# Kernel optimization log

Hardware: AMD Instinct MI355X
Metric: run time of the kernel (lower is better)

Reference implementation:

```python
import jax, jax.numpy as jnp
import numpy as np

N_HOS, N_TYPES = 8, 16
N_COMBOS = N_HOS * N_TYPES          # 128
N_STRUCTS = 512
BATCH = 2048
HID = 20
N_ITERS = 60                        # PDHG iterations (fixed, jit-friendly)
CONTROL = 10.0                      # control_strength in the original module


def _spectral_bound(S):
    # ||[S; I]||_2^2 = lambda_max(S^T S + I) via power iteration (S is constant).
    v = jnp.ones((S.shape[1],), S.dtype)
    def pit(v, _):
        u = S.T @ (S @ v) + v
        return u / jnp.linalg.norm(u), None
    v, _ = jax.lax.scan(pit, v, None, length=30)
    return jnp.sqrt(v @ (S.T @ (S @ v) + v))


def _solve_lp(S, b, z):
    """Batched solve of: max 1^T x - CONTROL*||x - z||_2  s.t. x >= 0, S x <= b.
    Chambolle-Pock PDHG with K = [S; -I], f(x) = -1^T x + CONTROL*||x - z||.
    S: [m, n]; b: [B, m]; z: [B, n] -> x: [B, n].
    """
    B, m = b.shape
    n = z.shape[1]
    L = _spectral_bound(S)
    tau = 0.9 / L
    sig = 0.9 / L
    w = jnp.ones((n,), z.dtype)     # LP objective weights (module uses ones)

    x = jnp.maximum(z, 0.0)
    xb = x
    lam1 = jnp.zeros((B, m), z.dtype)   # duals for S x <= b
    lam2 = jnp.zeros((B, n), z.dtype)   # duals for x >= 0 (lam2 <= 0 form)

    def step(carry, _):
        x, xb, lam1, lam2 = carry
        # dual ascent: prox of conjugates of the constraint indicators
        u1 = lam1 + sig * (xb @ S.T)                 # [B, m]
        lam1 = jnp.maximum(u1 - sig * b, 0.0)
        lam2 = jnp.minimum(lam2 + sig * xb, 0.0)
        # primal: prox of tau*(-w^T x + CONTROL*||x - z||): block soft-threshold
        v = x - tau * (lam1 @ S + lam2)
        u = v + tau * w - z
        nrm = jnp.linalg.norm(u, axis=1, keepdims=True)
        scale = jnp.maximum(0.0, 1.0 - tau * CONTROL / jnp.maximum(nrm, 1e-12))
        x_new = z + scale * u
        xb = 2.0 * x_new - x
        return (x_new, xb, lam1, lam2), None

    (x, _, _, _), _ = jax.lax.scan(step, (x, xb, lam1, lam2), None, length=N_ITERS)
    return x


def _mlp(Xf, W1, b1, W2, b2, W3, b3, W4, b4):
    h = jnp.tanh(Xf @ W1 + b1)
    h = jnp.tanh(h @ W2 + b2)
    h = jnp.tanh(h @ W3 + b3)
    return h @ W4 + b4


def setup_inputs() -> dict:
    key = jax.random.key(0)
    ks = jax.random.split(key, 10)
    X = jax.random.uniform(ks[0], (BATCH, N_HOS, N_TYPES), jnp.float32)
    # 0/1 cycle-incidence matrix, ~4 nonzeros per column (cycles of length ~4)
    S = jax.random.bernoulli(ks[1], 4.0 / N_COMBOS, (N_COMBOS, N_STRUCTS)).astype(jnp.float32)
    def lin(k, fi, fo):
        return jax.random.normal(k, (fi, fo), jnp.float32) / jnp.sqrt(fi)
    W1 = lin(ks[2], N_COMBOS, HID); b1 = jnp.zeros((HID,), jnp.float32)
    W2 = lin(ks[3], HID, HID);      b2 = jnp.zeros((HID,), jnp.float32)
    W3 = lin(ks[4], HID, HID);      b3 = jnp.zeros((HID,), jnp.float32)
    W4 = lin(ks[5], HID, N_STRUCTS); b4 = jnp.zeros((N_STRUCTS,), jnp.float32)
    return {"X": X, "W1": W1, "b1": b1, "W2": W2, "b2": b2, "W3": W3,
            "b3": b3, "W4": W4, "b4": b4, "S": S, "batch_size": BATCH}


def reference(X, W1, b1, W2, b2, W3, b3, W4, b4, S, batch_size):
    Xf = X.reshape(batch_size, N_COMBOS)       # bids, also the LP rhs b
    z = _mlp(Xf, W1, b1, W2, b2, W3, b3, W4, b4)   # [B, n_structures]
    return _solve_lp(S, Xf, z)                 # allocation x1 [B, n_structures]
```

## Files before the change

### kernel.cpp

```cpp
#include <hip/hip_runtime.h>


#define NC    128
#define NS    512
#define BATCH 2048
#define HID   20

typedef unsigned int  uint;
typedef unsigned short ushort;
typedef float v2f __attribute__((ext_vector_type(2)));


template <int CTRL, int RMASK = 0xf>
__device__ __forceinline__ float dppadd(float s) {
    return s + __builtin_bit_cast(float,
        __builtin_amdgcn_update_dpp(0, __builtin_bit_cast(int, s), CTRL, RMASK, 0xf, true));
}
__device__ __forceinline__ float quad_sum(float s) {
    s = dppadd<0xB1>(s);
    s = dppadd<0x4E>(s);
    return s;
}
__device__ __forceinline__ float wave_sum_bcast(float x) {
    float s = x;
    s = dppadd<0x111>(s);
    s = dppadd<0x112>(s);
    s = dppadd<0x114>(s);
    s = dppadd<0x118>(s);
    s = dppadd<0x142, 0xa>(s);
    s = dppadd<0x143, 0xc>(s);
    return __builtin_bit_cast(float, __builtin_amdgcn_readlane(__builtin_bit_cast(int, s), 63));
}
__device__ __forceinline__ v2f vfma(v2f a, v2f b, v2f c) { return __builtin_elementwise_fma(a, b, c); }
__device__ __forceinline__ v2f vmax0(v2f a) { const v2f z = {0.f, 0.f}; return __builtin_elementwise_max(a, z); }
__device__ __forceinline__ v2f vmin0(v2f a) { const v2f z = {0.f, 0.f}; return __builtin_elementwise_min(a, z); }

__global__ __launch_bounds__(512) void prep_scan(
    const float* __restrict__ S, uint* __restrict__ colmask_g, uint* __restrict__ rowbits_g)
{
    __shared__ uint mcol[NS];
    const int t = threadIdx.x, g = blockIdx.x;
    float vals[32];
#pragma unroll
    for (int j = 0; j < 32; ++j) vals[j] = S[(g * 32 + j) * NS + t];
    uint m = 0;
#pragma unroll
    for (int j = 0; j < 32; ++j) if (vals[j] != 0.0f) m |= (1u << j);
    mcol[t] = m;
    colmask_g[t * 4 + g] = m;
    __syncthreads();
    const int j = t >> 4, w = t & 15;
    uint val = 0;
#pragma unroll
    for (int c = 0; c < 32; ++c)
        val |= (((mcol[w * 32 + c] >> j) & 1u) << c);
    rowbits_g[(g * 32 + j) * 16 + w] = val;
}

__global__ __launch_bounds__(512) void prep_finish(
    const uint* __restrict__ colmask_g, const uint* __restrict__ rowbits_g,
    float* __restrict__ tau_ws,
    uint* __restrict__ col_meta, uint* __restrict__ col_cnt_g,
    uint* __restrict__ row_meta, uint* __restrict__ row_cnt_g)
{
    __shared__ ushort clist[NS][16];
    __shared__ ushort rql[NS][10];
    __shared__ int    ccnt_l[NS];
    __shared__ int    rcnt_l[NS];
    __shared__ float  u_lds[NS + 1];
    __shared__ float  sv_lds[NC];
    __shared__ float  red_pi[32];
    const int t = threadIdx.x;

    uint cm[4];
    { const uint4 c4 = *(const uint4*)&colmask_g[t * 4];
      cm[0] = c4.x; cm[1] = c4.y; cm[2] = c4.z; cm[3] = c4.w; }
    {
        int cc = 0;
#pragma unroll
        for (int g = 0; g < 4; ++g) {
            uint m = cm[g];
            while (m) {
                const int b = __ffs(m) - 1; m &= m - 1;
                if (cc < 16) clist[t][cc] = (ushort)((g * 32 + b) * 8);
                ++cc;
            }
        }
        if (cc > 16) cc = 16;
        const int cc2 = (cc + 1) & ~1;
        for (int k = cc; k < 16; ++k) clist[t][k] = (ushort)(NC * 8);
        ccnt_l[t] = cc2;
    }
    if (t < NC) {
#pragma unroll
        for (int q = 0; q < 4; ++q)
            for (int p = 0; p < 10; ++p) rql[t * 4 + q][p] = (ushort)(NS * 8);
        uint rb[16];
        { const uint4 a = *(const uint4*)&rowbits_g[t * 16];
          const uint4 b = *(const uint4*)&rowbits_g[t * 16 + 4];
          const uint4 c = *(const uint4*)&rowbits_g[t * 16 + 8];
          const uint4 d = *(const uint4*)&rowbits_g[t * 16 + 12];
          rb[0]=a.x; rb[1]=a.y; rb[2]=a.z;  rb[3]=a.w;  rb[4]=b.x;  rb[5]=b.y;  rb[6]=b.z;  rb[7]=b.w;
          rb[8]=c.x; rb[9]=c.y; rb[10]=c.z; rb[11]=c.w; rb[12]=d.x; rb[13]=d.y; rb[14]=d.z; rb[15]=d.w; }
        int e = 0;
#pragma unroll
        for (int w = 0; w < 16; ++w) {
            uint m = rb[w];
            while (m) {
                const int b = __ffs(m) - 1; m &= m - 1;
                const int q = e & 3, p = e >> 2;
                if (p < 10) rql[t * 4 + q][p] = (ushort)((w * 32 + b) * 8);
                ++e;
            }
        }
#pragma unroll
        for (int q = 0; q < 4; ++q) {
            int n = (e - q + 3) >> 2;
            if (n < 0) n = 0;
            if (n > 10) n = 10;
            rcnt_l[t * 4 + q] = (n + 1) & ~1;
        }
    }
    if (t == 0) u_lds[NS] = 0.0f;
    if (t < 32) red_pi[t] = 0.0f;
    u_lds[t] = 1.0f;
    __syncthreads();

    {
        col_cnt_g[t] = (uint)ccnt_l[t];
#pragma unroll
        for (int k = 0; k < 16; ++k) col_meta[t * 16 + k] = (uint)clist[t][k];
        row_cnt_g[t] = (uint)rcnt_l[t];
#pragma unroll
        for (int k = 0; k < 12; ++k)
            row_meta[t * 12 + k] = (k < 10) ? (uint)rql[t][k] : (uint)(NS * 8);
    }

    const int rcn = rcnt_l[t];
    float u_loc = 1.0f;
    for (int it = 0; it <= 30; ++it) {
        const float inv = it ? rsqrtf(red_pi[it - 1]) : 1.0f;
        float s = 0.0f;
        for (int k = 0; k < rcn; ++k) {
            const uint a = rql[t][k];
            s += *(const float*)((const char*)u_lds + (a >> 1));
        }
        s = quad_sum(s * inv);
        if ((t & 3) == 3) sv_lds[t >> 2] = s;
        __syncthreads();
        const float vt = u_loc * inv;
        float w = vt;
#pragma unroll
        for (int g = 0; g < 4; ++g) {
            uint m = cm[g];
            while (m) { const int b = __ffs(m) - 1; m &= m - 1; w += sv_lds[g * 32 + b]; }
        }
        float p = (it < 30) ? w * w : w * vt;
        p = wave_sum_bcast(p);
        if ((t & 63) == 0) atomicAdd(&red_pi[it], p);
        u_lds[t] = w;
        u_loc = w;
        __syncthreads();
    }
    if (t == 0) tau_ws[0] = 0.9f / sqrtf(red_pi[30]);
}

__global__ __launch_bounds__(512, 8) void solve_kernel(
    const float* __restrict__ X,
    const float* __restrict__ W1, const float* __restrict__ b1,
    const float* __restrict__ W2, const float* __restrict__ b2,
    const float* __restrict__ W3, const float* __restrict__ b3,
    const float* __restrict__ W4, const float* __restrict__ b4,
    const float* __restrict__ tau_ws,
    const uint* __restrict__ col_meta, const uint* __restrict__ col_cnt_g,
    const uint* __restrict__ row_meta, const uint* __restrict__ row_cnt_g,
    float* __restrict__ out)
{
    __shared__ alignas(16) float2 xb_lds[NS + 1];
    __shared__ alignas(16) float2 lam1_lds[NC + 1];
    __shared__ alignas(16) float2 redslot[8];
    __shared__ alignas(16) float2 b_lds[NC];
    __shared__ float ha[2][HID], hb[2][HID];

    const int t  = threadIdx.x;
    const int r0 = blockIdx.x * 2, r1 = r0 + 1;

    uint4 cA, cB, cC, cD, rA, rB, rC;
    { const uint4* g = (const uint4*)&col_meta[t * 16];
      cA = g[0]; cB = g[1]; cC = g[2]; cD = g[3]; }
    { const uint4* g = (const uint4*)&row_meta[t * 12];
      rA = g[0]; rB = g[1]; rC = g[2]; }
    const int ccn = (int)col_cnt_g[t];
    const int rcn = (int)row_cnt_g[t];

    if (t == 0) { xb_lds[NS] = make_float2(0.f, 0.f); lam1_lds[NC] = make_float2(0.f, 0.f); }
    if (t < NC) b_lds[t] = make_float2(X[r0 * NC + t], X[r1 * NC + t]);
    __syncthreads();

    if (t < 2 * HID) {
        const int rr = t >= HID, tt = t - rr * HID;
        float s = b1[tt];
        for (int k = 0; k < NC; ++k)
            s = fmaf(rr ? b_lds[k].y : b_lds[k].x, W1[k * HID + tt], s);
        ha[rr][tt] = tanhf(s);
    }
    __syncthreads();
    if (t < 2 * HID) {
        const int rr = t >= HID, tt = t - rr * HID;
        float s = b2[tt];
        for (int k = 0; k < HID; ++k) s = fmaf(ha[rr][k], W2[k * HID + tt], s);
        hb[rr][tt] = tanhf(s);
    }
    __syncthreads();
    if (t < 2 * HID) {
        const int rr = t >= HID, tt = t - rr * HID;
        float s = b3[tt];
        for (int k = 0; k < HID; ++k) s = fmaf(hb[rr][k], W3[k * HID + tt], s);
        ha[rr][tt] = tanhf(s);
    }
    __syncthreads();
    float z0 = b4[t], z1 = z0;
    for (int h = 0; h < HID; ++h) {
        const float w = W4[h * NS + t];
        z0 = fmaf(ha[0][h], w, z0);
        z1 = fmaf(ha[1][h], w, z1);
    }

    const float tau = tau_ws[0];
    const float c10 = 10.0f * tau;
    const v2f tauv = {tau, tau};
    const v2f sigv = tauv;
    const int r = t >> 2, q = t & 3;
    const v2f bb = {b_lds[r].x, b_lds[r].y};

    const v2f z = {z0, z1};
    v2f x  = vmax0(z);
    v2f xb = x;
    v2f u  = {0.f, 0.f};
    v2f l1 = {0.f, 0.f};
    v2f l2 = vmin0(sigv * xb);
    xb_lds[t] = make_float2(xb.x, xb.y);
    __syncthreads();

    const char* xbB = (const char*)xb_lds;
    const char* lmB = (const char*)lam1_lds;
    for (int it = 0; it < 60; ++it) {
        v2f s = {0.f, 0.f};
        s += *(const v2f*)(xbB + rA.x);
        s += *(const v2f*)(xbB + rA.y);
        if (rcn > 2) {
            s += *(const v2f*)(xbB + rA.z);
            s += *(const v2f*)(xbB + rA.w);
            if (rcn > 4) {
                s += *(const v2f*)(xbB + rB.x);
                s += *(const v2f*)(xbB + rB.y);
                if (rcn > 6) {
                    s += *(const v2f*)(xbB + rB.z);
                    s += *(const v2f*)(xbB + rB.w);
                    if (rcn > 8) {
                        s += *(const v2f*)(xbB + rC.x);
                        s += *(const v2f*)(xbB + rC.y);
                    }
                }
            }
        }
        const v2f sq = {quad_sum(s.x), quad_sum(s.y)};
        l1 = vmax0(vfma(sigv, sq - bb, l1));
        if (q == 3) lam1_lds[r] = make_float2(l1.x, l1.y);
        __syncthreads();
        v2f s2 = {0.f, 0.f};
        s2 += *(const v2f*)(lmB + cA.x);
        s2 += *(const v2f*)(lmB + cA.y);
        if (ccn > 2) {
            s2 += *(const v2f*)(lmB + cA.z);
            s2 += *(const v2f*)(lmB + cA.w);
            if (ccn > 4) {
                s2 += *(const v2f*)(lmB + cB.x);
                s2 += *(const v2f*)(lmB + cB.y);
                if (ccn > 6) {
                    s2 += *(const v2f*)(lmB + cB.z);
                    s2 += *(const v2f*)(lmB + cB.w);
                    if (ccn > 8) {
                        s2 += *(const v2f*)(lmB + cC.x);
                        s2 += *(const v2f*)(lmB + cC.y);
                        if (ccn > 10) {
                            s2 += *(const v2f*)(lmB + cC.z);
                            s2 += *(const v2f*)(lmB + cC.w);
                            if (ccn > 12) {
                                s2 += *(const v2f*)(lmB + cD.x);
                                s2 += *(const v2f*)(lmB + cD.y);
                                if (ccn > 14) {
                                    s2 += *(const v2f*)(lmB + cD.z);
                                    s2 += *(const v2f*)(lmB + cD.w);
                                }
                            }
                        }
                    }
                }
            }
        }
        const v2f v = x - tauv * (s2 + l2);
        u = (v + tauv) - z;
        const v2f p = u * u;
        const float p0 = wave_sum_bcast(p.x);
        const float p1 = wave_sum_bcast(p.y);
        if ((t & 63) == 0) redslot[t >> 6] = make_float2(p0, p1);
        __syncthreads();
        const float4* rs = (const float4*)redslot;
        const float4 Ra = rs[0], Rb = rs[1], Rc = rs[2], Rd = rs[3];
        const v2f tot = (((v2f){Ra.x, Ra.y} + (v2f){Ra.z, Ra.w}) +
                         ((v2f){Rb.x, Rb.y} + (v2f){Rb.z, Rb.w})) +
                        (((v2f){Rc.x, Rc.y} + (v2f){Rc.z, Rc.w}) +
                         ((v2f){Rd.x, Rd.y} + (v2f){Rd.z, Rd.w}));
        const v2f sc = {fmaxf(0.f, 1.f - c10 * rsqrtf(tot.x)),
                        fmaxf(0.f, 1.f - c10 * rsqrtf(tot.y))};
        const v2f xn = vfma(sc, u, z);
        xb = (xn + xn) - x;
        x  = xn;
        l2 = vmin0(vfma(sigv, xb, l2));
        xb_lds[t] = make_float2(xb.x, xb.y);
        __syncthreads();
    }
    out[r0 * NS + t] = x.x;
    out[r1 * NS + t] = x.y;
}

extern "C" void kernel_launch(void* const* d_in, const int* in_sizes, int n_in,
                              void* d_out, int out_size, void* d_ws, size_t ws_size,
                              hipStream_t stream)
{
    const float* X  = (const float*)d_in[0];
    const float* W1 = (const float*)d_in[1];
    const float* b1 = (const float*)d_in[2];
    const float* W2 = (const float*)d_in[3];
    const float* b2 = (const float*)d_in[4];
    const float* W3 = (const float*)d_in[5];
    const float* b3 = (const float*)d_in[6];
    const float* W4 = (const float*)d_in[7];
    const float* b4 = (const float*)d_in[8];
    const float* S  = (const float*)d_in[9];
    float* out = (float*)d_out;

    char* ws = (char*)d_ws;
    float* tau_ws    = (float*)(ws + 0);
    uint*  colmask_g = (uint*)(ws + 64);
    uint*  rowbits_g = (uint*)(ws + 8256);
    uint*  col_meta  = (uint*)(ws + 16448);
    uint*  col_cnt_g = (uint*)(ws + 49216);
    uint*  row_meta  = (uint*)(ws + 51264);
    uint*  row_cnt_g = (uint*)(ws + 75840);

    prep_scan<<<4, 512, 0, stream>>>(S, colmask_g, rowbits_g);
    prep_finish<<<1, 512, 0, stream>>>(colmask_g, rowbits_g, tau_ws,
                                       col_meta, col_cnt_g, row_meta, row_cnt_g);
    solve_kernel<<<BATCH / 2, 512, 0, stream>>>(X, W1, b1, W2, b2, W3, b3, W4, b4,
                                                tau_ws, col_meta, col_cnt_g,
                                                row_meta, row_cnt_g, out);
}
```

Measured before the change: 280.1 us.

## Process four batch rows per block with float4 LDS gathers and padded layout

The solve kernel now handles four batch rows per 512-thread block instead of two. Each thread carries v4f state, so every gathered LDS index and every barrier is amortized over twice as many rows, and the launch uses half as many blocks. The LDS arrays are padded (one slot per 8 entries) and the byte offsets are re-encoded at 16-byte stride, likely to reduce bank conflicts on the wider loads. In exchange, register use roughly doubles, the occupancy hint drops from 8 to 4 blocks per CU, and the grid shrinks to 512 blocks, which leaves less parallelism for hiding latency.

```diff
diff --git a/kernel.cpp b/kernel.cpp
--- a/kernel.cpp
+++ b/kernel.cpp
@@ -8,7 +8,7 @@
 
 typedef unsigned int  uint;
 typedef unsigned short ushort;
-typedef float v2f __attribute__((ext_vector_type(2)));
+typedef float v4f __attribute__((ext_vector_type(4)));
 
 
 template <int CTRL, int RMASK = 0xf>
@@ -31,9 +31,12 @@
     s = dppadd<0x143, 0xc>(s);
     return __builtin_bit_cast(float, __builtin_amdgcn_readlane(__builtin_bit_cast(int, s), 63));
 }
-__device__ __forceinline__ v2f vfma(v2f a, v2f b, v2f c) { return __builtin_elementwise_fma(a, b, c); }
-__device__ __forceinline__ v2f vmax0(v2f a) { const v2f z = {0.f, 0.f}; return __builtin_elementwise_max(a, z); }
-__device__ __forceinline__ v2f vmin0(v2f a) { const v2f z = {0.f, 0.f}; return __builtin_elementwise_min(a, z); }
+__device__ __forceinline__ v4f quad_sum4(v4f s) {
+    return (v4f){quad_sum(s.x), quad_sum(s.y), quad_sum(s.z), quad_sum(s.w)};
+}
+__device__ __forceinline__ v4f vfma(v4f a, v4f b, v4f c) { return __builtin_elementwise_fma(a, b, c); }
+__device__ __forceinline__ v4f vmax0(v4f a) { const v4f z = {0.f,0.f,0.f,0.f}; return __builtin_elementwise_max(a, z); }
+__device__ __forceinline__ v4f vmin0(v4f a) { const v4f z = {0.f,0.f,0.f,0.f}; return __builtin_elementwise_min(a, z); }
 
 __global__ __launch_bounds__(512) void prep_scan(
     const float* __restrict__ S, uint* __restrict__ colmask_g, uint* __restrict__ rowbits_g)
@@ -67,7 +70,7 @@
     __shared__ ushort rql[NS][10];
     __shared__ int    ccnt_l[NS];
     __shared__ int    rcnt_l[NS];
-    __shared__ float  u_lds[NS + 1];
+    __shared__ float  u_lds[577];
     __shared__ float  sv_lds[NC];
     __shared__ float  red_pi[32];
     const int t = threadIdx.x;
@@ -82,19 +85,20 @@
             uint m = cm[g];
             while (m) {
                 const int b = __ffs(m) - 1; m &= m - 1;
-                if (cc < 16) clist[t][cc] = (ushort)((g * 32 + b) * 8);
+                const int i = g * 32 + b;
+                if (cc < 16) clist[t][cc] = (ushort)((i + (i >> 3)) * 16);
                 ++cc;
             }
         }
         if (cc > 16) cc = 16;
         const int cc2 = (cc + 1) & ~1;
-        for (int k = cc; k < 16; ++k) clist[t][k] = (ushort)(NC * 8);
+        for (int k = cc; k < 16; ++k) clist[t][k] = (ushort)(144 * 16);
         ccnt_l[t] = cc2;
     }
     if (t < NC) {
 #pragma unroll
         for (int q = 0; q < 4; ++q)
-            for (int p = 0; p < 10; ++p) rql[t * 4 + q][p] = (ushort)(NS * 8);
+            for (int p = 0; p < 10; ++p) rql[t * 4 + q][p] = (ushort)(576 * 16);
         uint rb[16];
         { const uint4 a = *(const uint4*)&rowbits_g[t * 16];
           const uint4 b = *(const uint4*)&rowbits_g[t * 16 + 4];
@@ -109,7 +113,8 @@
             while (m) {
                 const int b = __ffs(m) - 1; m &= m - 1;
                 const int q = e & 3, p = e >> 2;
-                if (p < 10) rql[t * 4 + q][p] = (ushort)((w * 32 + b) * 8);
+                const int j = w * 32 + b;
+                if (p < 10) rql[t * 4 + q][p] = (ushort)((j + (j >> 3)) * 16);
                 ++e;
             }
         }
@@ -121,9 +126,9 @@
             rcnt_l[t * 4 + q] = (n + 1) & ~1;
         }
     }
-    if (t == 0) u_lds[NS] = 0.0f;
+    if (t == 0) u_lds[576] = 0.0f;
     if (t < 32) red_pi[t] = 0.0f;
-    u_lds[t] = 1.0f;
+    u_lds[t + (t >> 3)] = 1.0f;
     __syncthreads();
 
     {
@@ -133,7 +138,7 @@
         row_cnt_g[t] = (uint)rcnt_l[t];
 #pragma unroll
         for (int k = 0; k < 12; ++k)
-            row_meta[t * 12 + k] = (k < 10) ? (uint)rql[t][k] : (uint)(NS * 8);
+            row_meta[t * 12 + k] = (k < 10) ? (uint)rql[t][k] : (uint)(576 * 16);
     }
 
     const int rcn = rcnt_l[t];
@@ -143,7 +148,7 @@
         float s = 0.0f;
         for (int k = 0; k < rcn; ++k) {
             const uint a = rql[t][k];
-            s += *(const float*)((const char*)u_lds + (a >> 1));
+            s += *(const float*)((const char*)u_lds + (a >> 2));
         }
         s = quad_sum(s * inv);
         if ((t & 3) == 3) sv_lds[t >> 2] = s;
@@ -158,14 +163,14 @@
         float p = (it < 30) ? w * w : w * vt;
         p = wave_sum_bcast(p);
         if ((t & 63) == 0) atomicAdd(&red_pi[it], p);
-        u_lds[t] = w;
+        u_lds[t + (t >> 3)] = w;
         u_loc = w;
         __syncthreads();
     }
     if (t == 0) tau_ws[0] = 0.9f / sqrtf(red_pi[30]);
 }
 
-__global__ __launch_bounds__(512, 8) void solve_kernel(
+__global__ __launch_bounds__(512, 4) void solve_kernel(
     const float* __restrict__ X,
     const float* __restrict__ W1, const float* __restrict__ b1,
     const float* __restrict__ W2, const float* __restrict__ b2,
@@ -176,14 +181,14 @@
     const uint* __restrict__ row_meta, const uint* __restrict__ row_cnt_g,
     float* __restrict__ out)
 {
-    __shared__ alignas(16) float2 xb_lds[NS + 1];
-    __shared__ alignas(16) float2 lam1_lds[NC + 1];
-    __shared__ alignas(16) float2 redslot[8];
-    __shared__ alignas(16) float2 b_lds[NC];
-    __shared__ float ha[2][HID], hb[2][HID];
+    __shared__ alignas(16) v4f xb_lds[577];
+    __shared__ alignas(16) v4f lam1_lds[145];
+    __shared__ alignas(16) v4f redslot[8];
+    __shared__ alignas(16) v4f b_lds[NC];
+    __shared__ float ha[4][HID], hb[4][HID];
 
     const int t  = threadIdx.x;
-    const int r0 = blockIdx.x * 2, r1 = r0 + 1;
+    const int r0 = blockIdx.x * 4;
 
     uint4 cA, cB, cC, cD, rA, rB, rC;
     { const uint4* g = (const uint4*)&col_meta[t * 16];
@@ -193,105 +198,114 @@
     const int ccn = (int)col_cnt_g[t];
     const int rcn = (int)row_cnt_g[t];
 
-    if (t == 0) { xb_lds[NS] = make_float2(0.f, 0.f); lam1_lds[NC] = make_float2(0.f, 0.f); }
-    if (t < NC) b_lds[t] = make_float2(X[r0 * NC + t], X[r1 * NC + t]);
-    __syncthreads();
-
-    if (t < 2 * HID) {
-        const int rr = t >= HID, tt = t - rr * HID;
+    if (t == 0) {
+        xb_lds[576]   = (v4f){0.f, 0.f, 0.f, 0.f};
+        lam1_lds[144] = (v4f){0.f, 0.f, 0.f, 0.f};
+    }
+    if (t < NC)
+        b_lds[t] = (v4f){X[r0 * NC + t],       X[(r0 + 1) * NC + t],
+                         X[(r0 + 2) * NC + t], X[(r0 + 3) * NC + t]};
+    __syncthreads();
+
+    if (t < 4 * HID) {
+        const int rr = t / HID, tt = t - rr * HID;
         float s = b1[tt];
-        for (int k = 0; k < NC; ++k)
-            s = fmaf(rr ? b_lds[k].y : b_lds[k].x, W1[k * HID + tt], s);
+        for (int k = 0; k < NC; ++k) s = fmaf(b_lds[k][rr], W1[k * HID + tt], s);
         ha[rr][tt] = tanhf(s);
     }
     __syncthreads();
-    if (t < 2 * HID) {
-        const int rr = t >= HID, tt = t - rr * HID;
+    if (t < 4 * HID) {
+        const int rr = t / HID, tt = t - rr * HID;
         float s = b2[tt];
         for (int k = 0; k < HID; ++k) s = fmaf(ha[rr][k], W2[k * HID + tt], s);
         hb[rr][tt] = tanhf(s);
     }
     __syncthreads();
-    if (t < 2 * HID) {
-        const int rr = t >= HID, tt = t - rr * HID;
+    if (t < 4 * HID) {
+        const int rr = t / HID, tt = t - rr * HID;
         float s = b3[tt];
         for (int k = 0; k < HID; ++k) s = fmaf(hb[rr][k], W3[k * HID + tt], s);
         ha[rr][tt] = tanhf(s);
     }
     __syncthreads();
-    float z0 = b4[t], z1 = z0;
-    for (int h = 0; h < HID; ++h) {
-        const float w = W4[h * NS + t];
-        z0 = fmaf(ha[0][h], w, z0);
-        z1 = fmaf(ha[1][h], w, z1);
+    v4f z;
+    {
+        const float bz = b4[t];
+        z = (v4f){bz, bz, bz, bz};
+        for (int h = 0; h < HID; ++h) {
+            const float w = W4[h * NS + t];
+            const v4f hv = {ha[0][h], ha[1][h], ha[2][h], ha[3][h]};
+            z = vfma(hv, (v4f){w, w, w, w}, z);
+        }
     }
 
     const float tau = tau_ws[0];
     const float c10 = 10.0f * tau;
-    const v2f tauv = {tau, tau};
-    const v2f sigv = tauv;
+    const v4f tauv = {tau, tau, tau, tau};
+    const v4f sigv = tauv;
     const int r = t >> 2, q = t & 3;
-    const v2f bb = {b_lds[r].x, b_lds[r].y};
-
-    const v2f z = {z0, z1};
-    v2f x  = vmax0(z);
-    v2f xb = x;
-    v2f u  = {0.f, 0.f};
-    v2f l1 = {0.f, 0.f};
-    v2f l2 = vmin0(sigv * xb);
-    xb_lds[t] = make_float2(xb.x, xb.y);
+    const int pub = t + (t >> 3);
+    const int pir = r + (r >> 3);
+    const v4f bb = b_lds[r];
+
+    v4f x  = vmax0(z);
+    v4f xb = x;
+    v4f u  = {0.f, 0.f, 0.f, 0.f};
+    v4f l1 = {0.f, 0.f, 0.f, 0.f};
+    v4f l2 = vmin0(sigv * xb);
+    xb_lds[pub] = xb;
     __syncthreads();
 
     const char* xbB = (const char*)xb_lds;
     const char* lmB = (const char*)lam1_lds;
     for (int it = 0; it < 60; ++it) {
-        v2f s = {0.f, 0.f};
-        s += *(const v2f*)(xbB + rA.x);
-        s += *(const v2f*)(xbB + rA.y);
+        v4f s = {0.f, 0.f, 0.f, 0.f};
+        s += *(const v4f*)(xbB + rA.x);
+        s += *(const v4f*)(xbB + rA.y);
         if (rcn > 2) {
-            s += *(const v2f*)(xbB + rA.z);
-            s += *(const v2f*)(xbB + rA.w);
+            s += *(const v4f*)(xbB + rA.z);
+            s += *(const v4f*)(xbB + rA.w);
             if (rcn > 4) {
-                s += *(const v2f*)(xbB + rB.x);
-                s += *(const v2f*)(xbB + rB.y);
+                s += *(const v4f*)(xbB + rB.x);
+                s += *(const v4f*)(xbB + rB.y);
                 if (rcn > 6) {
-                    s += *(const v2f*)(xbB + rB.z);
-                    s += *(const v2f*)(xbB + rB.w);
+                    s += *(const v4f*)(xbB + rB.z);
+                    s += *(const v4f*)(xbB + rB.w);
                     if (rcn > 8) {
-                        s += *(const v2f*)(xbB + rC.x);
-                        s += *(const v2f*)(xbB + rC.y);
+                        s += *(const v4f*)(xbB + rC.x);
+                        s += *(const v4f*)(xbB + rC.y);
                     }
                 }
             }
         }
-        const v2f sq = {quad_sum(s.x), quad_sum(s.y)};
+        const v4f sq = quad_sum4(s);
         l1 = vmax0(vfma(sigv, sq - bb, l1));
-        if (q == 3) lam1_lds[r] = make_float2(l1.x, l1.y);
-        __syncthreads();
-        v2f s2 = {0.f, 0.f};
-        s2 += *(const v2f*)(lmB + cA.x);
-        s2 += *(const v2f*)(lmB + cA.y);
+        if (q == 3) lam1_lds[pir] = l1;
+        __syncthreads();
+        v4f s2 = {0.f, 0.f, 0.f, 0.f};
+        s2 += *(const v4f*)(lmB + cA.x);
+        s2 += *(const v4f*)(lmB + cA.y);
         if (ccn > 2) {
-            s2 += *(const v2f*)(lmB + cA.z);
-            s2 += *(const v2f*)(lmB + cA.w);
+            s2 += *(const v4f*)(lmB + cA.z);
+            s2 += *(const v4f*)(lmB + cA.w);
             if (ccn > 4) {
-                s2 += *(const v2f*)(lmB + cB.x);
-                s2 += *(const v2f*)(lmB + cB.y);
+                s2 += *(const v4f*)(lmB + cB.x);
+                s2 += *(const v4f*)(lmB + cB.y);
                 if (ccn > 6) {
-                    s2 += *(const v2f*)(lmB + cB.z);
-                    s2 += *(const v2f*)(lmB + cB.w);
+                    s2 += *(const v4f*)(lmB + cB.z);
+                    s2 += *(const v4f*)(lmB + cB.w);
                     if (ccn > 8) {
-                        s2 += *(const v2f*)(lmB + cC.x);
-                        s2 += *(const v2f*)(lmB + cC.y);
+                        s2 += *(const v4f*)(lmB + cC.x);
+                        s2 += *(const v4f*)(lmB + cC.y);
                         if (ccn > 10) {
-                            s2 += *(const v2f*)(lmB + cC.z);
-                            s2 += *(const v2f*)(lmB + cC.w);
+                            s2 += *(const v4f*)(lmB + cC.z);
+                            s2 += *(const v4f*)(lmB + cC.w);
                             if (ccn > 12) {
-                                s2 += *(const v2f*)(lmB + cD.x);
-                                s2 += *(const v2f*)(lmB + cD.y);
+                                s2 += *(const v4f*)(lmB + cD.x);
+                                s2 += *(const v4f*)(lmB + cD.y);
                                 if (ccn > 14) {
-                                    s2 += *(const v2f*)(lmB + cD.z);
-                                    s2 += *(const v2f*)(lmB + cD.w);
+                                    s2 += *(const v4f*)(lmB + cD.z);
+                                    s2 += *(const v4f*)(lmB + cD.w);
                                 }
                             }
                         }
@@ -299,30 +313,30 @@
                 }
             }
         }
-        const v2f v = x - tauv * (s2 + l2);
+        const v4f v = x - tauv * (s2 + l2);
         u = (v + tauv) - z;
-        const v2f p = u * u;
-        const float p0 = wave_sum_bcast(p.x);
-        const float p1 = wave_sum_bcast(p.y);
-        if ((t & 63) == 0) redslot[t >> 6] = make_float2(p0, p1);
-        __syncthreads();
-        const float4* rs = (const float4*)redslot;
-        const float4 Ra = rs[0], Rb = rs[1], Rc = rs[2], Rd = rs[3];
-        const v2f tot = (((v2f){Ra.x, Ra.y} + (v2f){Ra.z, Ra.w}) +
-                         ((v2f){Rb.x, Rb.y} + (v2f){Rb.z, Rb.w})) +
-                        (((v2f){Rc.x, Rc.y} + (v2f){Rc.z, Rc.w}) +
-                         ((v2f){Rd.x, Rd.y} + (v2f){Rd.z, Rd.w}));
-        const v2f sc = {fmaxf(0.f, 1.f - c10 * rsqrtf(tot.x)),
-                        fmaxf(0.f, 1.f - c10 * rsqrtf(tot.y))};
-        const v2f xn = vfma(sc, u, z);
+        const v4f p = u * u;
+        const v4f ps = {wave_sum_bcast(p.x), wave_sum_bcast(p.y),
+                        wave_sum_bcast(p.z), wave_sum_bcast(p.w)};
+        if ((t & 63) == 0) redslot[t >> 6] = ps;
+        __syncthreads();
+        const v4f tot = ((redslot[0] + redslot[1]) + (redslot[2] + redslot[3])) +
+                        ((redslot[4] + redslot[5]) + (redslot[6] + redslot[7]));
+        const v4f sc = {fmaxf(0.f, 1.f - c10 * rsqrtf(tot.x)),
+                        fmaxf(0.f, 1.f - c10 * rsqrtf(tot.y)),
+                        fmaxf(0.f, 1.f - c10 * rsqrtf(tot.z)),
+                        fmaxf(0.f, 1.f - c10 * rsqrtf(tot.w))};
+        const v4f xn = vfma(sc, u, z);
         xb = (xn + xn) - x;
         x  = xn;
         l2 = vmin0(vfma(sigv, xb, l2));
-        xb_lds[t] = make_float2(xb.x, xb.y);
-        __syncthreads();
-    }
-    out[r0 * NS + t] = x.x;
-    out[r1 * NS + t] = x.y;
+        xb_lds[pub] = xb;
+        __syncthreads();
+    }
+    out[r0 * NS + t]       = x.x;
+    out[(r0 + 1) * NS + t] = x.y;
+    out[(r0 + 2) * NS + t] = x.z;
+    out[(r0 + 3) * NS + t] = x.w;
 }
 
 extern "C" void kernel_launch(void* const* d_in, const int* in_sizes, int n_in,
@@ -353,7 +367,7 @@
     prep_scan<<<4, 512, 0, stream>>>(S, colmask_g, rowbits_g);
     prep_finish<<<1, 512, 0, stream>>>(colmask_g, rowbits_g, tau_ws,
                                        col_meta, col_cnt_g, row_meta, row_cnt_g);
-    solve_kernel<<<BATCH / 2, 512, 0, stream>>>(X, W1, b1, W2, b2, W3, b3, W4, b4,
+    solve_kernel<<<BATCH / 4, 512, 0, stream>>>(X, W1, b1, W2, b2, W3, b3, W4, b4,
                                                 tau_ws, col_meta, col_cnt_g,
                                                 row_meta, row_cnt_g, out);
 }
```

Measured after the change: 269.8 us. 1.04x faster.
